# Kernel optimization log

Measured on AMD Instinct MI355X. Metric: run time of the kernel, lower is better.

The kernel has to match this reference:

```python
import jax, jax.numpy as jnp
import numpy as np

N_NODES = 200000
N_EDGES = 3200000
F_IN = 16
N_CLASSES = 16


def setup_inputs() -> dict:
    key = jax.random.key(0)
    ks = jax.random.split(key, 8)
    s = 1.0 / np.sqrt(F_IN)
    return {
        "x": jax.random.normal(ks[0], (N_NODES, F_IN), dtype=jnp.float32),
        "edge_index": jax.random.randint(ks[1], (2, N_EDGES), 0, N_NODES, dtype=jnp.int32),
        "eps1": jnp.zeros((), dtype=jnp.float32),
        "w1a": jax.random.normal(ks[2], (F_IN, 16), dtype=jnp.float32) * s,
        "b1a": jnp.zeros((16,), dtype=jnp.float32),
        "w1b": jax.random.normal(ks[3], (16, 16), dtype=jnp.float32) * 0.25,
        "b1b": jnp.zeros((16,), dtype=jnp.float32),
        "eps2": jnp.zeros((), dtype=jnp.float32),
        "w2a": jax.random.normal(ks[4], (16, N_CLASSES), dtype=jnp.float32) * 0.25,
        "b2a": jnp.zeros((N_CLASSES,), dtype=jnp.float32),
        "w2b": jax.random.normal(ks[5], (N_CLASSES, N_CLASSES), dtype=jnp.float32) * 0.25,
        "b2b": jnp.zeros((N_CLASSES,), dtype=jnp.float32),
    }


def _gin_conv(x, src, dst, eps, wa, ba, wb, bb, n_nodes):
    # sum aggregation of source-node features into destination nodes
    agg = jax.ops.segment_sum(x[src], dst, num_segments=n_nodes)  # [N, F]
    h = (1.0 + eps) * x + agg
    # 2-layer MLP: Linear -> ReLU -> Linear
    h = jax.nn.relu(h @ wa + ba) @ wb + bb
    return h


def reference(x, edge_index, eps1, w1a, b1a, w1b, b1b, eps2, w2a, b2a, w2b, b2b):
    src, dst = edge_index[0], edge_index[1]
    n = x.shape[0]
    h = jax.nn.relu(_gin_conv(x, src, dst, eps1, w1a, b1a, w1b, b1b, n))
    # F.dropout with training=False is identity (module assumed in eval mode)
    h = _gin_conv(h, src, dst, eps2, w2a, b2a, w2b, b2b, n)
    return jax.nn.log_softmax(h, axis=1)
```

## Files before the change

### kernel.cpp

```cpp
#include <hip/hip_runtime.h>

#define N_NODES 200000
#define N_EDGES 3200000
#define F 16
#define NB 782
#define NB_PAD 832
#define EPB 8192
#define EBLOCKS ((N_EDGES + EPB - 1) / EPB)
#define ET 1024
#define CAP 5120
#define GIN_NODES 64
#define GIN_BLOCKS ((N_NODES + GIN_NODES - 1) / GIN_NODES)


__device__ __forceinline__ unsigned bf16pack2(float lo, float hi) {
    unsigned ul = __float_as_uint(lo);
    unsigned uh = __float_as_uint(hi);
    ul = (ul + 0x7fffu + ((ul >> 16) & 1u)) >> 16;
    uh = (uh + 0x7fffu + ((uh >> 16) & 1u)) >> 16;
    return ul | (uh << 16);
}
#define BLO(w) __uint_as_float((w) << 16)
#define BHI(w) __uint_as_float((w) & 0xffff0000u)

__device__ __forceinline__ void acc8(uint4 w0, uint4 w1, float acc[16]) {
    acc[0]  += BLO(w0.x); acc[1]  += BHI(w0.x);
    acc[2]  += BLO(w0.y); acc[3]  += BHI(w0.y);
    acc[4]  += BLO(w0.z); acc[5]  += BHI(w0.z);
    acc[6]  += BLO(w0.w); acc[7]  += BHI(w0.w);
    acc[8]  += BLO(w1.x); acc[9]  += BHI(w1.x);
    acc[10] += BLO(w1.y); acc[11] += BHI(w1.y);
    acc[12] += BLO(w1.z); acc[13] += BHI(w1.z);
    acc[14] += BLO(w1.w); acc[15] += BHI(w1.w);
}


__global__ __launch_bounds__(256) void conv_bf16(const float* __restrict__ x,
                                                 unsigned* __restrict__ xb) {
    int i = blockIdx.x * blockDim.x + threadIdx.x;
    if (i >= N_NODES * F / 8) return;
    const float4* p = (const float4*)(x + (size_t)i * 8);
    float4 a = p[0], b = p[1];
    uint4 r;
    r.x = bf16pack2(a.x, a.y);
    r.y = bf16pack2(a.z, a.w);
    r.z = bf16pack2(b.x, b.y);
    r.w = bf16pack2(b.z, b.w);
    ((uint4*)xb)[i] = r;
}


__global__ __launch_bounds__(ET) void count_kernel(const int* __restrict__ dst,
                                                   int* __restrict__ cntmat) {
    __shared__ int lh[NB];
    const int t = threadIdx.x;
    for (int i = t; i < NB; i += ET) lh[i] = 0;
    __syncthreads();

    const int base4 = blockIdx.x * (EPB / 4);
    #pragma unroll
    for (int k = 0; k < EPB / 4 / ET; ++k) {
        int i4 = base4 + k * ET + t;
        if (i4 < N_EDGES / 4) {
            int4 d = *(const int4*)(dst + i4 * 4);
            atomicAdd(&lh[d.x >> 8], 1);
            atomicAdd(&lh[d.y >> 8], 1);
            atomicAdd(&lh[d.z >> 8], 1);
            atomicAdd(&lh[d.w >> 8], 1);
        }
    }
    __syncthreads();
    int* row = cntmat + (size_t)blockIdx.x * NB_PAD;
    for (int i = t; i < NB; i += ET) row[i] = lh[i];
}


__global__ __launch_bounds__(512) void colscan(int* __restrict__ cntmat,
                                               int* __restrict__ bcnt) {
    __shared__ int part[512];
    const int t = threadIdx.x;
    const int b = blockIdx.x;
    int v = 0;
    if (t < EBLOCKS) v = cntmat[(size_t)t * NB_PAD + b];
    part[t] = v;
    __syncthreads();
    for (int off = 1; off < 512; off <<= 1) {
        int o = (t >= off) ? part[t - off] : 0;
        __syncthreads();
        part[t] += o;
        __syncthreads();
    }
    if (t < EBLOCKS) cntmat[(size_t)t * NB_PAD + b] = part[t] - v;
    if (t == EBLOCKS - 1) bcnt[b] = part[t];
}


__global__ __launch_bounds__(1024) void bucket_scan(const int* __restrict__ bcnt,
                                                    int* __restrict__ bbase) {
    __shared__ int part[1024];
    const int t = threadIdx.x;
    int v = (t < NB) ? bcnt[t] : 0;
    part[t] = v;
    __syncthreads();
    for (int off = 1; off < 1024; off <<= 1) {
        int other = (t >= off) ? part[t - off] : 0;
        __syncthreads();
        part[t] += other;
        __syncthreads();
    }
    if (t < NB) bbase[t] = part[t] - v;
    if (t == 1023) bbase[NB] = part[1023];
}


__global__ __launch_bounds__(ET) void partition2(const int* __restrict__ src,
                                                 const int* __restrict__ dst,
                                                 const int* __restrict__ bbase,
                                                 const int* __restrict__ cntmat,
                                                 int* __restrict__ ebuf) {
    __shared__ int lh[NB];
    __shared__ int sbase[NB];
    const int t = threadIdx.x;
    const int* row = cntmat + (size_t)blockIdx.x * NB_PAD;
    for (int i = t; i < NB; i += ET) {
        sbase[i] = bbase[i] + row[i];
        lh[i] = 0;
    }
    __syncthreads();

    const int base4 = blockIdx.x * (EPB / 4);
    #pragma unroll
    for (int k = 0; k < EPB / 4 / ET; ++k) {
        int i4 = base4 + k * ET + t;
        if (i4 < N_EDGES / 4) {
            int4 s = *(const int4*)(src + i4 * 4);
            int4 d = *(const int4*)(dst + i4 * 4);
            int b, p;
            b = d.x >> 8; p = atomicAdd(&lh[b], 1); ebuf[sbase[b] + p] = (s.x << 8) | (d.x & 255);
            b = d.y >> 8; p = atomicAdd(&lh[b], 1); ebuf[sbase[b] + p] = (s.y << 8) | (d.y & 255);
            b = d.z >> 8; p = atomicAdd(&lh[b], 1); ebuf[sbase[b] + p] = (s.z << 8) | (d.z & 255);
            b = d.w >> 8; p = atomicAdd(&lh[b], 1); ebuf[sbase[b] + p] = (s.w << 8) | (d.w & 255);
        }
    }
}


__global__ __launch_bounds__(256) void sort_csr(const int* __restrict__ bbase,
                                                int* __restrict__ ebuf,
                                                int* __restrict__ noffs,
                                                int* __restrict__ scratch) {
    __shared__ int srec[CAP];
    __shared__ int hist[256];
    __shared__ int lofs[256];
    const int t = threadIdx.x;
    const int b = blockIdx.x;
    hist[t] = 0;
    __syncthreads();

    const int beg = bbase[b];
    const int end = bbase[b + 1];
    const int sz = end - beg;
    const int n = b * 256 + t;

    for (int k = beg + t; k < end; k += 256)
        atomicAdd(&hist[ebuf[k] & 255], 1);
    __syncthreads();
    int v = hist[t];
    lofs[t] = v;
    __syncthreads();
    for (int off = 1; off < 256; off <<= 1) {
        int o = (t >= off) ? lofs[t - off] : 0;
        __syncthreads();
        lofs[t] += o;
        __syncthreads();
    }
    const int myend = lofs[t];
    const int mybeg = myend - v;
    __syncthreads();
    hist[t] = mybeg;
    __syncthreads();

    if (sz <= CAP) {
        for (int k = beg + t; k < end; k += 256) {
            int rec = ebuf[k];
            int p = atomicAdd(&hist[rec & 255], 1);
            srec[p] = rec >> 8;
        }
        __syncthreads();
        for (int k = t; k < sz; k += 256) ebuf[beg + k] = srec[k];
    } else {
        for (int k = beg + t; k < end; k += 256) scratch[k] = ebuf[k];
        __syncthreads();
        for (int k = beg + t; k < end; k += 256) {
            int rec = scratch[k];
            int p = atomicAdd(&hist[rec & 255], 1);
            ebuf[beg + p] = rec >> 8;
        }
    }

    if (n < N_NODES) noffs[n] = beg + mybeg;
    if (b == 0 && t == 0) noffs[N_NODES] = N_EDGES;
}


template <bool LAYER2>
__global__ __launch_bounds__(256) void gin_gather(
    const unsigned short* __restrict__ xin,
    const int* __restrict__ noffs,
    const int* __restrict__ ebuf,
    const float* __restrict__ epsp,
    const float* __restrict__ wa, const float* __restrict__ ba,
    const float* __restrict__ wb, const float* __restrict__ bb,
    void* __restrict__ outp) {
    __shared__ float swa[256], swb[256], sba[16], sbb[16];
    const int t = threadIdx.x;
    swa[t] = wa[t];
    swb[t] = wb[t];
    if (t < 16) { sba[t] = ba[t]; sbb[t] = bb[t]; }
    __syncthreads();

    const int n = blockIdx.x * GIN_NODES + (t >> 2);
    const int sub = t & 3;
    if (n >= N_NODES) return;

    const int beg = noffs[n];
    const int end = noffs[n + 1];

    float acc[16];
    #pragma unroll
    for (int q = 0; q < 16; ++q) acc[q] = 0.0f;

    int k = beg + sub;
    for (; k + 12 < end; k += 16) {
        int s0 = ebuf[k];
        int s1 = ebuf[k + 4];
        int s2 = ebuf[k + 8];
        int s3 = ebuf[k + 12];
        const uint4* r0 = (const uint4*)(xin + (size_t)s0 * F);
        const uint4* r1 = (const uint4*)(xin + (size_t)s1 * F);
        const uint4* r2 = (const uint4*)(xin + (size_t)s2 * F);
        const uint4* r3 = (const uint4*)(xin + (size_t)s3 * F);
        uint4 a0 = r0[0], a1 = r0[1];
        uint4 b0 = r1[0], b1 = r1[1];
        uint4 c0 = r2[0], c1 = r2[1];
        uint4 d0 = r3[0], d1 = r3[1];
        acc8(a0, a1, acc);
        acc8(b0, b1, acc);
        acc8(c0, c1, acc);
        acc8(d0, d1, acc);
    }
    for (; k + 4 < end; k += 8) {
        int s0 = ebuf[k];
        int s1 = ebuf[k + 4];
        const uint4* r0 = (const uint4*)(xin + (size_t)s0 * F);
        const uint4* r1 = (const uint4*)(xin + (size_t)s1 * F);
        uint4 a0 = r0[0], a1 = r0[1];
        uint4 b0 = r1[0], b1 = r1[1];
        acc8(a0, a1, acc);
        acc8(b0, b1, acc);
    }
    if (k < end) {
        const uint4* r0 = (const uint4*)(xin + (size_t)ebuf[k] * F);
        acc8(r0[0], r0[1], acc);
    }

    #pragma unroll
    for (int q = 0; q < 16; ++q) {
        acc[q] += __shfl_xor(acc[q], 1);
        acc[q] += __shfl_xor(acc[q], 2);
    }
    if (sub != 0) return;

    const float eps = 1.0f + *epsp;
    const uint4* xr = (const uint4*)(xin + (size_t)n * F);
    uint4 w0 = xr[0], w1 = xr[1];
    float h[16];
    h[0]  = fmaf(eps, BLO(w0.x), acc[0]);   h[1]  = fmaf(eps, BHI(w0.x), acc[1]);
    h[2]  = fmaf(eps, BLO(w0.y), acc[2]);   h[3]  = fmaf(eps, BHI(w0.y), acc[3]);
    h[4]  = fmaf(eps, BLO(w0.z), acc[4]);   h[5]  = fmaf(eps, BHI(w0.z), acc[5]);
    h[6]  = fmaf(eps, BLO(w0.w), acc[6]);   h[7]  = fmaf(eps, BHI(w0.w), acc[7]);
    h[8]  = fmaf(eps, BLO(w1.x), acc[8]);   h[9]  = fmaf(eps, BHI(w1.x), acc[9]);
    h[10] = fmaf(eps, BLO(w1.y), acc[10]);  h[11] = fmaf(eps, BHI(w1.y), acc[11]);
    h[12] = fmaf(eps, BLO(w1.z), acc[12]);  h[13] = fmaf(eps, BHI(w1.z), acc[13]);
    h[14] = fmaf(eps, BLO(w1.w), acc[14]);  h[15] = fmaf(eps, BHI(w1.w), acc[15]);

    float m[16];
    #pragma unroll
    for (int jj = 0; jj < 16; ++jj) {
        float a = sba[jj];
        #pragma unroll
        for (int i = 0; i < 16; ++i) a = fmaf(h[i], swa[i * 16 + jj], a);
        m[jj] = fmaxf(a, 0.0f);
    }

    float o[16];
    #pragma unroll
    for (int jj = 0; jj < 16; ++jj) {
        float a = sbb[jj];
        #pragma unroll
        for (int i = 0; i < 16; ++i) a = fmaf(m[i], swb[i * 16 + jj], a);
        o[jj] = LAYER2 ? a : fmaxf(a, 0.0f);
    }

    if (LAYER2) {
        float mx = o[0];
        #pragma unroll
        for (int jj = 1; jj < 16; ++jj) mx = fmaxf(mx, o[jj]);
        float s = 0.0f;
        #pragma unroll
        for (int jj = 0; jj < 16; ++jj) s += expf(o[jj] - mx);
        float lse = mx + logf(s);
        float* orow = (float*)outp + (size_t)n * F;
        #pragma unroll
        for (int q = 0; q < 4; ++q) {
            ((float4*)orow)[q] = make_float4(o[q * 4 + 0] - lse, o[q * 4 + 1] - lse,
                                             o[q * 4 + 2] - lse, o[q * 4 + 3] - lse);
        }
    } else {
        unsigned* orow = (unsigned*)outp + (size_t)n * 8;
        uint4 r0, r1;
        r0.x = bf16pack2(o[0],  o[1]);   r0.y = bf16pack2(o[2],  o[3]);
        r0.z = bf16pack2(o[4],  o[5]);   r0.w = bf16pack2(o[6],  o[7]);
        r1.x = bf16pack2(o[8],  o[9]);   r1.y = bf16pack2(o[10], o[11]);
        r1.z = bf16pack2(o[12], o[13]);  r1.w = bf16pack2(o[14], o[15]);
        ((uint4*)orow)[0] = r0;
        ((uint4*)orow)[1] = r1;
    }
}


__global__ __launch_bounds__(256) void scatter_kernel(
    const float* __restrict__ feat,
    const int* __restrict__ src,
    const int* __restrict__ dst,
    float* __restrict__ agg) {
    int e = blockIdx.x * blockDim.x + threadIdx.x;
    if (e >= N_EDGES) return;
    int s = src[e];
    int d = dst[e];
    const float4* fs = (const float4*)(feat + (size_t)s * F);
    float* ad = agg + (size_t)d * F;
    #pragma unroll
    for (int q = 0; q < 4; ++q) {
        float4 v = fs[q];
        atomicAdd(ad + q * 4 + 0, v.x);
        atomicAdd(ad + q * 4 + 1, v.y);
        atomicAdd(ad + q * 4 + 2, v.z);
        atomicAdd(ad + q * 4 + 3, v.w);
    }
}

template <bool RELU_OUT, bool LOGSOFTMAX>
__global__ __launch_bounds__(256) void mlp_kernel(
    const float* __restrict__ xin,
    const float* __restrict__ agg,
    const float* __restrict__ epsp,
    const float* __restrict__ wa, const float* __restrict__ ba,
    const float* __restrict__ wb, const float* __restrict__ bb,
    float* __restrict__ out) {
    __shared__ float swa[256], swb[256], sba[16], sbb[16];
    int t = threadIdx.x;
    swa[t] = wa[t];
    swb[t] = wb[t];
    if (t < 16) { sba[t] = ba[t]; sbb[t] = bb[t]; }
    __syncthreads();

    int n = blockIdx.x * blockDim.x + t;
    if (n >= N_NODES) return;

    float eps = 1.0f + *epsp;
    const float4* xr = (const float4*)(xin + (size_t)n * F);
    const float4* ar = (const float4*)(agg + (size_t)n * F);
    float h[16];
    #pragma unroll
    for (int q = 0; q < 4; ++q) {
        float4 xv = xr[q];
        float4 av = ar[q];
        h[q * 4 + 0] = fmaf(eps, xv.x, av.x);
        h[q * 4 + 1] = fmaf(eps, xv.y, av.y);
        h[q * 4 + 2] = fmaf(eps, xv.z, av.z);
        h[q * 4 + 3] = fmaf(eps, xv.w, av.w);
    }

    float m[16];
    #pragma unroll
    for (int jj = 0; jj < 16; ++jj) {
        float a = sba[jj];
        #pragma unroll
        for (int i = 0; i < 16; ++i) a = fmaf(h[i], swa[i * 16 + jj], a);
        m[jj] = fmaxf(a, 0.0f);
    }

    float o[16];
    #pragma unroll
    for (int jj = 0; jj < 16; ++jj) {
        float a = sbb[jj];
        #pragma unroll
        for (int i = 0; i < 16; ++i) a = fmaf(m[i], swb[i * 16 + jj], a);
        o[jj] = RELU_OUT ? fmaxf(a, 0.0f) : a;
    }

    if (LOGSOFTMAX) {
        float mx = o[0];
        #pragma unroll
        for (int jj = 1; jj < 16; ++jj) mx = fmaxf(mx, o[jj]);
        float s = 0.0f;
        #pragma unroll
        for (int jj = 0; jj < 16; ++jj) s += expf(o[jj] - mx);
        float lse = mx + logf(s);
        #pragma unroll
        for (int jj = 0; jj < 16; ++jj) o[jj] -= lse;
    }

    float4* orow = (float4*)(out + (size_t)n * F);
    #pragma unroll
    for (int q = 0; q < 4; ++q) {
        orow[q] = make_float4(o[q * 4 + 0], o[q * 4 + 1], o[q * 4 + 2], o[q * 4 + 3]);
    }
}


extern "C" void kernel_launch(void* const* d_in, const int* in_sizes, int n_in,
                              void* d_out, int out_size, void* d_ws, size_t ws_size,
                              hipStream_t stream) {
    const float* x    = (const float*)d_in[0];
    const int*   ei   = (const int*)d_in[1];
    const float* eps1 = (const float*)d_in[2];
    const float* w1a  = (const float*)d_in[3];
    const float* b1a  = (const float*)d_in[4];
    const float* w1b  = (const float*)d_in[5];
    const float* b1b  = (const float*)d_in[6];
    const float* eps2 = (const float*)d_in[7];
    const float* w2a  = (const float*)d_in[8];
    const float* b2a  = (const float*)d_in[9];
    const float* w2b  = (const float*)d_in[10];
    const float* b2b  = (const float*)d_in[11];

    float* out = (float*)d_out;
    const int* src = ei;
    const int* dst = ei + N_EDGES;

    size_t off_bcnt   = 0;
    size_t off_bbase  = off_bcnt + (size_t)NB_PAD * 4;
    size_t off_noffs  = off_bbase + (size_t)NB_PAD * 4;
    size_t off_ebuf   = off_noffs + ((size_t)N_NODES + 64) * 4;
    size_t off_xb     = off_ebuf + (size_t)N_EDGES * 4;
    size_t off_hb     = off_xb + (size_t)N_NODES * F * 2;
    size_t off_cnt    = off_hb + (size_t)N_NODES * F * 2;
    size_t need       = off_cnt + (size_t)EBLOCKS * NB_PAD * 4;

    if (ws_size >= need) {
        int*            bcnt   = (int*)((char*)d_ws + off_bcnt);
        int*            bbase  = (int*)((char*)d_ws + off_bbase);
        int*            noffs  = (int*)((char*)d_ws + off_noffs);
        int*            ebuf   = (int*)((char*)d_ws + off_ebuf);
        unsigned short* xb     = (unsigned short*)((char*)d_ws + off_xb);
        unsigned short* hb     = (unsigned short*)((char*)d_ws + off_hb);
        int*            cntmat = (int*)((char*)d_ws + off_cnt);

        count_kernel<<<EBLOCKS, ET, 0, stream>>>(dst, cntmat);
        conv_bf16<<<(N_NODES * F / 8 + 255) / 256, 256, 0, stream>>>(x, (unsigned*)xb);
        colscan<<<NB, 512, 0, stream>>>(cntmat, bcnt);
        bucket_scan<<<1, 1024, 0, stream>>>(bcnt, bbase);
        partition2<<<EBLOCKS, ET, 0, stream>>>(src, dst, bbase, cntmat, ebuf);
        sort_csr<<<NB, 256, 0, stream>>>(bbase, ebuf, noffs, (int*)d_out);

        gin_gather<false><<<GIN_BLOCKS, 256, 0, stream>>>(
            xb, noffs, ebuf, eps1, w1a, b1a, w1b, b1b, hb);
        gin_gather<true><<<GIN_BLOCKS, 256, 0, stream>>>(
            hb, noffs, ebuf, eps2, w2a, b2a, w2b, b2b, out);
    } else {
        float* agg = (float*)d_ws;
        const int edge_blocks = (N_EDGES + 255) / 256;
        const int node_blocks = (N_NODES + 255) / 256;
        const size_t agg_bytes = (size_t)N_NODES * F * sizeof(float);

        hipMemsetAsync(agg, 0, agg_bytes, stream);
        scatter_kernel<<<edge_blocks, 256, 0, stream>>>(x, src, dst, agg);
        mlp_kernel<true, false><<<node_blocks, 256, 0, stream>>>(
            x, agg, eps1, w1a, b1a, w1b, b1b, out);

        hipMemsetAsync(agg, 0, agg_bytes, stream);
        scatter_kernel<<<edge_blocks, 256, 0, stream>>>(out, src, dst, agg);
        mlp_kernel<false, true><<<node_blocks, 256, 0, stream>>>(
            out, agg, eps2, w2a, b2a, w2b, b2b, out);
    }
}
```

Measured before the change: 148.6 us.

## Split each node's edges by source half and use nontemporal index loads

The sort kernel now bins edges by destination and by whether the source index falls in the lower or upper half of the node range. It records a per-node midpoint so the gather walks the lower-half sources first and then the upper-half ones, aiming for better cache locality on the feature gather. Edge-index and ebuf loads switch to nontemporal loads to reduce cache pollution, and EPB is doubled. The sort block size grows to 512 threads, and the extra midpoint array adds one more read per node plus another loop tail in the gather.

Result: slower. 178.6 us (+20.1%).

```diff
diff --git a/kernel.cpp b/kernel.cpp
--- a/kernel.cpp
+++ b/kernel.cpp
@@ -5,13 +5,24 @@
 #define F 16
 #define NB 782
 #define NB_PAD 832
-#define EPB 8192
+#define EPB 16384
 #define EBLOCKS ((N_EDGES + EPB - 1) / EPB)
 #define ET 1024
 #define CAP 5120
+#define SORT_T 512
+#define SPLIT 100000
 #define GIN_NODES 64
 #define GIN_BLOCKS ((N_NODES + GIN_NODES - 1) / GIN_NODES)
 
+
+typedef int iv4 __attribute__((ext_vector_type(4)));
+
+__device__ __forceinline__ int ntload(const int* p) {
+    return __builtin_nontemporal_load(p);
+}
+__device__ __forceinline__ iv4 ntload4(const int* p) {
+    return __builtin_nontemporal_load((const iv4*)p);
+}
 
 __device__ __forceinline__ unsigned bf16pack2(float lo, float hi) {
     unsigned ul = __float_as_uint(lo);
@@ -32,6 +43,42 @@
     acc[10] += BLO(w1.y); acc[11] += BHI(w1.y);
     acc[12] += BLO(w1.z); acc[13] += BHI(w1.z);
     acc[14] += BLO(w1.w); acc[15] += BHI(w1.w);
+}
+
+__device__ __forceinline__ void gather_range(
+    const unsigned short* __restrict__ xin,
+    const int* __restrict__ ebuf,
+    int lo, int hi, int sub, float acc[16]) {
+    int k = lo + sub;
+    for (; k + 12 < hi; k += 16) {
+        int s0 = ntload(ebuf + k);
+        int s1 = ntload(ebuf + k + 4);
+        int s2 = ntload(ebuf + k + 8);
+        int s3 = ntload(ebuf + k + 12);
+        const uint4* r0 = (const uint4*)(xin + (size_t)s0 * F);
+        const uint4* r1 = (const uint4*)(xin + (size_t)s1 * F);
+        const uint4* r2 = (const uint4*)(xin + (size_t)s2 * F);
+        const uint4* r3 = (const uint4*)(xin + (size_t)s3 * F);
+        uint4 a0 = r0[0], a1 = r0[1];
+        uint4 b0 = r1[0], b1 = r1[1];
+        uint4 c0 = r2[0], c1 = r2[1];
+        uint4 d0 = r3[0], d1 = r3[1];
+        acc8(a0, a1, acc); acc8(b0, b1, acc);
+        acc8(c0, c1, acc); acc8(d0, d1, acc);
+    }
+    for (; k + 4 < hi; k += 8) {
+        int s0 = ntload(ebuf + k);
+        int s1 = ntload(ebuf + k + 4);
+        const uint4* r0 = (const uint4*)(xin + (size_t)s0 * F);
+        const uint4* r1 = (const uint4*)(xin + (size_t)s1 * F);
+        uint4 a0 = r0[0], a1 = r0[1];
+        uint4 b0 = r1[0], b1 = r1[1];
+        acc8(a0, a1, acc); acc8(b0, b1, acc);
+    }
+    if (k < hi) {
+        const uint4* r0 = (const uint4*)(xin + (size_t)ntload(ebuf + k) * F);
+        acc8(r0[0], r0[1], acc);
+    }
 }
 
 
@@ -62,7 +109,7 @@
     for (int k = 0; k < EPB / 4 / ET; ++k) {
         int i4 = base4 + k * ET + t;
         if (i4 < N_EDGES / 4) {
-            int4 d = *(const int4*)(dst + i4 * 4);
+            iv4 d = ntload4(dst + i4 * 4);
             atomicAdd(&lh[d.x >> 8], 1);
             atomicAdd(&lh[d.y >> 8], 1);
             atomicAdd(&lh[d.z >> 8], 1);
@@ -133,8 +180,8 @@
     for (int k = 0; k < EPB / 4 / ET; ++k) {
         int i4 = base4 + k * ET + t;
         if (i4 < N_EDGES / 4) {
-            int4 s = *(const int4*)(src + i4 * 4);
-            int4 d = *(const int4*)(dst + i4 * 4);
+            iv4 s = ntload4(src + i4 * 4);
+            iv4 d = ntload4(dst + i4 * 4);
             int b, p;
             b = d.x >> 8; p = atomicAdd(&lh[b], 1); ebuf[sbase[b] + p] = (s.x << 8) | (d.x & 255);
             b = d.y >> 8; p = atomicAdd(&lh[b], 1); ebuf[sbase[b] + p] = (s.y << 8) | (d.y & 255);
@@ -145,13 +192,14 @@
 }
 
 
-__global__ __launch_bounds__(256) void sort_csr(const int* __restrict__ bbase,
-                                                int* __restrict__ ebuf,
-                                                int* __restrict__ noffs,
-                                                int* __restrict__ scratch) {
+__global__ __launch_bounds__(SORT_T) void sort_csr(const int* __restrict__ bbase,
+                                                   int* __restrict__ ebuf,
+                                                   int* __restrict__ noffs,
+                                                   int* __restrict__ nmid,
+                                                   int* __restrict__ scratch) {
     __shared__ int srec[CAP];
-    __shared__ int hist[256];
-    __shared__ int lofs[256];
+    __shared__ int hist[512];
+    __shared__ int lofs[512];
     const int t = threadIdx.x;
     const int b = blockIdx.x;
     hist[t] = 0;
@@ -160,15 +208,17 @@
     const int beg = bbase[b];
     const int end = bbase[b + 1];
     const int sz = end - beg;
-    const int n = b * 256 + t;
-
-    for (int k = beg + t; k < end; k += 256)
-        atomicAdd(&hist[ebuf[k] & 255], 1);
+
+    for (int k = beg + t; k < end; k += SORT_T) {
+        int rec = ntload(ebuf + k);
+        int bin = ((rec & 255) << 1) | ((rec >> 8) >= SPLIT);
+        atomicAdd(&hist[bin], 1);
+    }
     __syncthreads();
     int v = hist[t];
     lofs[t] = v;
     __syncthreads();
-    for (int off = 1; off < 256; off <<= 1) {
+    for (int off = 1; off < 512; off <<= 1) {
         int o = (t >= off) ? lofs[t - off] : 0;
         __syncthreads();
         lofs[t] += o;
@@ -181,24 +231,30 @@
     __syncthreads();
 
     if (sz <= CAP) {
-        for (int k = beg + t; k < end; k += 256) {
-            int rec = ebuf[k];
-            int p = atomicAdd(&hist[rec & 255], 1);
+        for (int k = beg + t; k < end; k += SORT_T) {
+            int rec = ntload(ebuf + k);
+            int bin = ((rec & 255) << 1) | ((rec >> 8) >= SPLIT);
+            int p = atomicAdd(&hist[bin], 1);
             srec[p] = rec >> 8;
         }
         __syncthreads();
-        for (int k = t; k < sz; k += 256) ebuf[beg + k] = srec[k];
+        for (int k = t; k < sz; k += SORT_T) ebuf[beg + k] = srec[k];
     } else {
-        for (int k = beg + t; k < end; k += 256) scratch[k] = ebuf[k];
-        __syncthreads();
-        for (int k = beg + t; k < end; k += 256) {
+        for (int k = beg + t; k < end; k += SORT_T) scratch[k] = ebuf[k];
+        __syncthreads();
+        for (int k = beg + t; k < end; k += SORT_T) {
             int rec = scratch[k];
-            int p = atomicAdd(&hist[rec & 255], 1);
+            int bin = ((rec & 255) << 1) | ((rec >> 8) >= SPLIT);
+            int p = atomicAdd(&hist[bin], 1);
             ebuf[beg + p] = rec >> 8;
         }
     }
 
-    if (n < N_NODES) noffs[n] = beg + mybeg;
+    const int n = b * 256 + (t >> 1);
+    if (n < N_NODES) {
+        if ((t & 1) == 0) noffs[n] = beg + mybeg;
+        else              nmid[n]  = beg + mybeg;
+    }
     if (b == 0 && t == 0) noffs[N_NODES] = N_EDGES;
 }
 
@@ -207,6 +263,7 @@
 __global__ __launch_bounds__(256) void gin_gather(
     const unsigned short* __restrict__ xin,
     const int* __restrict__ noffs,
+    const int* __restrict__ nmid,
     const int* __restrict__ ebuf,
     const float* __restrict__ epsp,
     const float* __restrict__ wa, const float* __restrict__ ba,
@@ -224,45 +281,15 @@
     if (n >= N_NODES) return;
 
     const int beg = noffs[n];
+    const int mid = nmid[n];
     const int end = noffs[n + 1];
 
     float acc[16];
     #pragma unroll
     for (int q = 0; q < 16; ++q) acc[q] = 0.0f;
 
-    int k = beg + sub;
-    for (; k + 12 < end; k += 16) {
-        int s0 = ebuf[k];
-        int s1 = ebuf[k + 4];
-        int s2 = ebuf[k + 8];
-        int s3 = ebuf[k + 12];
-        const uint4* r0 = (const uint4*)(xin + (size_t)s0 * F);
-        const uint4* r1 = (const uint4*)(xin + (size_t)s1 * F);
-        const uint4* r2 = (const uint4*)(xin + (size_t)s2 * F);
-        const uint4* r3 = (const uint4*)(xin + (size_t)s3 * F);
-        uint4 a0 = r0[0], a1 = r0[1];
-        uint4 b0 = r1[0], b1 = r1[1];
-        uint4 c0 = r2[0], c1 = r2[1];
-        uint4 d0 = r3[0], d1 = r3[1];
-        acc8(a0, a1, acc);
-        acc8(b0, b1, acc);
-        acc8(c0, c1, acc);
-        acc8(d0, d1, acc);
-    }
-    for (; k + 4 < end; k += 8) {
-        int s0 = ebuf[k];
-        int s1 = ebuf[k + 4];
-        const uint4* r0 = (const uint4*)(xin + (size_t)s0 * F);
-        const uint4* r1 = (const uint4*)(xin + (size_t)s1 * F);
-        uint4 a0 = r0[0], a1 = r0[1];
-        uint4 b0 = r1[0], b1 = r1[1];
-        acc8(a0, a1, acc);
-        acc8(b0, b1, acc);
-    }
-    if (k < end) {
-        const uint4* r0 = (const uint4*)(xin + (size_t)ebuf[k] * F);
-        acc8(r0[0], r0[1], acc);
-    }
+    gather_range(xin, ebuf, beg, mid, sub, acc);
+    gather_range(xin, ebuf, mid, end, sub, acc);
 
     #pragma unroll
     for (int q = 0; q < 16; ++q) {
@@ -443,7 +470,8 @@
     size_t off_bcnt   = 0;
     size_t off_bbase  = off_bcnt + (size_t)NB_PAD * 4;
     size_t off_noffs  = off_bbase + (size_t)NB_PAD * 4;
-    size_t off_ebuf   = off_noffs + ((size_t)N_NODES + 64) * 4;
+    size_t off_nmid   = off_noffs + ((size_t)N_NODES + 64) * 4;
+    size_t off_ebuf   = off_nmid + ((size_t)N_NODES + 64) * 4;
     size_t off_xb     = off_ebuf + (size_t)N_EDGES * 4;
     size_t off_hb     = off_xb + (size_t)N_NODES * F * 2;
     size_t off_cnt    = off_hb + (size_t)N_NODES * F * 2;
@@ -453,6 +481,7 @@
         int*            bcnt   = (int*)((char*)d_ws + off_bcnt);
         int*            bbase  = (int*)((char*)d_ws + off_bbase);
         int*            noffs  = (int*)((char*)d_ws + off_noffs);
+        int*            nmid   = (int*)((char*)d_ws + off_nmid);
         int*            ebuf   = (int*)((char*)d_ws + off_ebuf);
         unsigned short* xb     = (unsigned short*)((char*)d_ws + off_xb);
         unsigned short* hb     = (unsigned short*)((char*)d_ws + off_hb);
@@ -463,12 +492,12 @@
         colscan<<<NB, 512, 0, stream>>>(cntmat, bcnt);
         bucket_scan<<<1, 1024, 0, stream>>>(bcnt, bbase);
         partition2<<<EBLOCKS, ET, 0, stream>>>(src, dst, bbase, cntmat, ebuf);
-        sort_csr<<<NB, 256, 0, stream>>>(bbase, ebuf, noffs, (int*)d_out);
+        sort_csr<<<NB, SORT_T, 0, stream>>>(bbase, ebuf, noffs, nmid, (int*)d_out);
 
         gin_gather<false><<<GIN_BLOCKS, 256, 0, stream>>>(
-            xb, noffs, ebuf, eps1, w1a, b1a, w1b, b1b, hb);
+            xb, noffs, nmid, ebuf, eps1, w1a, b1a, w1b, b1b, hb);
         gin_gather<true><<<GIN_BLOCKS, 256, 0, stream>>>(
-            hb, noffs, ebuf, eps2, w2a, b2a, w2b, b2b, out);
+            hb, noffs, nmid, ebuf, eps2, w2a, b2a, w2b, b2b, out);
     } else {
         float* agg = (float*)d_ws;
         const int edge_blocks = (N_EDGES + 255) / 256;
```
